# Optimization experiments

Measured on AMD Instinct MI355X. Metric: run time of the kernel, lower is better.

## Reference

```python
import jax, jax.numpy as jnp
import numpy as np

EPS = 1.1920928955078125e-07  # torch fp32 default eps for F.rms_norm
N_HEADS = 16
HEAD_DIM = 128


def apply_rotary_emb(x, cos, sin):
    # x: [B,S,H,D]; cos/sin: [1,S,1,D/2]
    d = x.shape[-1] // 2
    x1, x2 = x[..., :d], x[..., d:]
    return jnp.concatenate([x1 * cos + x2 * sin, -x1 * sin + x2 * cos], axis=-1)


def rms_norm(x):
    # F.rms_norm over last dim, no learned weight
    ms = jnp.mean(jnp.square(x), axis=-1, keepdims=True)
    return x * jax.lax.rsqrt(ms + EPS)


def setup_inputs() -> dict:
    key = jax.random.key(0)
    ks = jax.random.split(key, 7)
    B, S, D = 2, 2048, 2048
    half = HEAD_DIM // 2
    # rotary tables (built like standard RoPE for realism)
    inv_freq = 1.0 / (10000.0 ** (np.arange(0, half, dtype=np.float32) / half))
    t = np.arange(S, dtype=np.float32)
    freqs = np.outer(t, inv_freq)  # [S, D/2]
    cos = jnp.asarray(np.cos(freqs))[None, :, None, :]
    sin = jnp.asarray(np.sin(freqs))[None, :, None, :]
    sd = 1.0 / np.sqrt(D)
    return {
        "x": jax.random.normal(ks[0], (B, S, D), jnp.float32),
        "cos": cos,
        "sin": sin,
        "Wq": jax.random.normal(ks[1], (D, D), jnp.float32) * sd,
        "Wk": jax.random.normal(ks[2], (D, D), jnp.float32) * sd,
        "Wv": jax.random.normal(ks[3], (D, D), jnp.float32) * sd,
        "Wo": jax.random.normal(ks[4], (D, D), jnp.float32) * sd,
    }


def reference(x, cos, sin, Wq, Wk, Wv, Wo):
    B, S, D = x.shape
    H, Hd = N_HEADS, HEAD_DIM
    q = (x @ Wq.T).reshape(B, S, H, Hd)
    k = (x @ Wk.T).reshape(B, S, H, Hd)
    v = (x @ Wv.T).reshape(B, S, H, Hd)
    q = apply_rotary_emb(q, cos[:, :S], sin[:, :S])
    k = apply_rotary_emb(k, cos[:, :S], sin[:, :S])
    q = rms_norm(q) * 1.2  # [B,S,H,Hd]
    k = rms_norm(k) * 1.2
    scale = 1.0 / jnp.sqrt(jnp.asarray(Hd, x.dtype))
    # scores: [B,H,Sq,Sk]
    scores = jnp.einsum("bqhd,bkhd->bhqk", q, k) * scale
    attn = jax.nn.softmax(scores, axis=-1)
    y = jnp.einsum("bhqk,bkhd->bqhd", attn, v).reshape(B, S, D)
    return y @ Wo.T
```

## Files before the change

kernel.cpp:

```cpp
#include <hip/hip_runtime.h>
#include <hip/hip_bf16.h>
#include <math.h>

typedef __bf16 bf16;
typedef __attribute__((ext_vector_type(8))) __bf16 bf16x8;
typedef __attribute__((ext_vector_type(4))) float f32x4;

#define DEV __device__ __forceinline__

DEV void gload16(const void* g, void* l) {
    __builtin_amdgcn_global_load_lds(
        (__attribute__((address_space(1))) void*)(void*)g,
        (__attribute__((address_space(3))) void*)l, 16, 0, 0);
}

DEV unsigned pk2(float a, float b) {
    union { bf16 h[2]; unsigned u; } z;
    z.h[0] = (bf16)a; z.h[1] = (bf16)b;
    return z.u;
}

__global__ __launch_bounds__(256) void cvt_kernel(const float* __restrict__ in,
                                                  bf16* __restrict__ out, int n8) {
    for (int i = blockIdx.x * 256 + threadIdx.x; i < n8; i += gridDim.x * 256) {
        const float4* p = (const float4*)(in + (size_t)i * 8);
        float4 a = p[0], b = p[1];
        bf16x8 o;
        o[0] = (bf16)a.x; o[1] = (bf16)a.y; o[2] = (bf16)a.z; o[3] = (bf16)a.w;
        o[4] = (bf16)b.x; o[5] = (bf16)b.y; o[6] = (bf16)b.z; o[7] = (bf16)b.w;
        *(bf16x8*)(out + (size_t)i * 8) = o;
    }
}

template <bool F32OUT>
__global__ __launch_bounds__(256) void gemm_bt(const bf16* __restrict__ A,
                                               const bf16* __restrict__ B,
                                               void* __restrict__ Cout,
                                               int M, int N, int K) {
    __shared__ __align__(16) bf16 As[128 * 64];
    __shared__ __align__(16) bf16 Bs[128 * 64];
    const int tid = threadIdx.x, lane = tid & 63, wv = tid >> 6;
    const int tm = blockIdx.y * 128, tn = blockIdx.x * 128;
    const int wr = (wv >> 1) * 64, wc = (wv & 1) * 64;

    f32x4 acc[4][4] = {};
    const int scb = (lane & 7) * 16;

    for (int k0 = 0; k0 < K; k0 += 64) {
#pragma unroll
        for (int i = 0; i < 4; ++i) {
            int chunk = wv * 4 + i;
            int row = chunk * 8 + (lane >> 3);
            int cb = scb ^ ((row & 7) << 4);
            gload16((const char*)(A + (size_t)(tm + row) * K + k0) + cb,
                    (char*)As + chunk * 1024);
            gload16((const char*)(B + (size_t)(tn + row) * K + k0) + cb,
                    (char*)Bs + chunk * 1024);
        }
        __syncthreads();
#pragma unroll
        for (int kk = 0; kk < 2; ++kk) {
            bf16x8 af[4], bfr[4];
#pragma unroll
            for (int m = 0; m < 4; ++m) {
                int row = wr + m * 16 + (lane & 15);
                int cb = (kk * 64 + ((lane >> 4) * 16)) ^ ((row & 7) << 4);
                af[m] = *(const bf16x8*)((const char*)As + row * 128 + cb);
            }
#pragma unroll
            for (int n = 0; n < 4; ++n) {
                int row = wc + n * 16 + (lane & 15);
                int cb = (kk * 64 + ((lane >> 4) * 16)) ^ ((row & 7) << 4);
                bfr[n] = *(const bf16x8*)((const char*)Bs + row * 128 + cb);
            }
#pragma unroll
            for (int m = 0; m < 4; ++m)
#pragma unroll
                for (int n = 0; n < 4; ++n)
                    acc[m][n] = __builtin_amdgcn_mfma_f32_16x16x32_bf16(
                        af[m], bfr[n], acc[m][n], 0, 0, 0);
        }
        __syncthreads();
    }
#pragma unroll
    for (int m = 0; m < 4; ++m)
#pragma unroll
        for (int n = 0; n < 4; ++n)
#pragma unroll
            for (int r = 0; r < 4; ++r) {
                int row = tm + wr + m * 16 + (lane >> 4) * 4 + r;
                int col = tn + wc + n * 16 + (lane & 15);
                if (F32OUT)
                    ((float*)Cout)[(size_t)row * N + col] = acc[m][n][r];
                else
                    ((bf16*)Cout)[(size_t)row * N + col] = (bf16)acc[m][n][r];
            }
}

__global__ __launch_bounds__(256) void rope_rms(bf16* __restrict__ q,
                                                bf16* __restrict__ k,
                                                const float* __restrict__ cosp,
                                                const float* __restrict__ sinp) {
    int gw = blockIdx.x * 4 + (threadIdx.x >> 6);
    int lane = threadIdx.x & 63;
    bf16* base = (blockIdx.y == 0) ? q : k;
    int m = gw >> 4, h = gw & 15;
    int s = m & 2047;
    bf16* p = base + (size_t)m * 2048 + h * 128;
    float x1 = (float)p[lane], x2 = (float)p[lane + 64];
    float c = cosp[s * 64 + lane], si = sinp[s * 64 + lane];
    float r1 = x1 * c + x2 * si;
    float r2 = x2 * c - x1 * si;
    float ss = r1 * r1 + r2 * r2;
#pragma unroll
    for (int msk = 1; msk < 64; msk <<= 1) ss += __shfl_xor(ss, msk);
    float sc = rsqrtf(ss * (1.0f / 128.0f) + 1.1920928955078125e-07f) * 1.2f;
    p[lane] = (bf16)(r1 * sc);
    p[lane + 64] = (bf16)(r2 * sc);
}

__global__ __launch_bounds__(512) void attn_kernel(const bf16* __restrict__ q,
                                                   const bf16* __restrict__ k,
                                                   const bf16* __restrict__ v,
                                                   bf16* __restrict__ y) {
    __shared__ __align__(16) bf16 Ks[64 * 128];
    __shared__ __align__(16) bf16 Vt[128][72];

    const int tid = threadIdx.x, lane = tid & 63, wv = tid >> 6;
    const int hi = lane >> 4, ql = lane & 15;

    int wgid = blockIdx.y * 16 + blockIdx.x;
    int xcd = wgid & 7, j = wgid >> 3;
    int bh = xcd * 4 + (j >> 4);
    int qblk = j & 15;
    const int b = bh >> 4, h = bh & 15;
    const int q0 = qblk * 128;

    const bf16* qrow = q + (size_t)(b * 2048 + q0 + wv * 16 + ql) * 2048 +
                       h * 128 + hi * 8;
    bf16x8 qf[4];
#pragma unroll
    for (int kk = 0; kk < 4; ++kk) qf[kk] = *(const bf16x8*)(qrow + kk * 32);

    float mrun = -INFINITY, lrun = 0.f;
    f32x4 acco[8] = {};

    const int dcol = lane + 64 * (wv & 1);
    const int kvg = wv >> 1;
    const bf16* vcol = v + (size_t)(b * 2048) * 2048 + h * 128 + dcol;

    const float scale = 0.08838834764831845f;

    for (int kt = 0; kt < 2048; kt += 64) {
#pragma unroll
        for (int i = 0; i < 2; ++i) {
            int chunk = wv * 2 + i;
            int row = chunk * 4 + hi;
            int cb = ((lane & 15) * 16) ^ ((row & 7) << 4);
            gload16((const char*)(k + (size_t)(b * 2048 + kt + row) * 2048 + h * 128) + cb,
                    (char*)Ks + chunk * 1024);
        }
        {
            const bf16* vp = vcol + (size_t)(kt + kvg * 16) * 2048;
            bf16x8 va, vb2;
#pragma unroll
            for (int jj = 0; jj < 8; ++jj) {
                va[jj] = vp[(size_t)jj * 2048];
                vb2[jj] = vp[(size_t)(jj + 8) * 2048];
            }
            *(bf16x8*)(&Vt[dcol][kvg * 16]) = va;
            *(bf16x8*)(&Vt[dcol][kvg * 16 + 8]) = vb2;
        }
        __syncthreads();

        f32x4 st[4];
#pragma unroll
        for (int kc = 0; kc < 4; ++kc) {
            f32x4 a = {};
#pragma unroll
            for (int kk = 0; kk < 4; ++kk) {
                int row = kc * 16 + ql;
                int cb = (kk * 64 + 16 * hi) ^ ((row & 7) << 4);
                const bf16x8 kf = *(const bf16x8*)((const char*)Ks + row * 256 + cb);
                a = __builtin_amdgcn_mfma_f32_16x16x32_bf16(kf, qf[kk], a, 0, 0, 0);
            }
            st[kc] = a;
        }

        float s[4][4], mx = -INFINITY;
#pragma unroll
        for (int kc = 0; kc < 4; ++kc)
#pragma unroll
            for (int r = 0; r < 4; ++r) {
                s[kc][r] = st[kc][r] * scale;
                mx = fmaxf(mx, s[kc][r]);
            }
        mx = fmaxf(mx, __shfl_xor(mx, 16));
        mx = fmaxf(mx, __shfl_xor(mx, 32));
        float mn = fmaxf(mrun, mx);
        float alpha = __expf(mrun - mn);
        mrun = mn;
        float p[4][4], rs = 0.f;
#pragma unroll
        for (int kc = 0; kc < 4; ++kc)
#pragma unroll
            for (int r = 0; r < 4; ++r) {
                p[kc][r] = __expf(s[kc][r] - mn);
                rs += p[kc][r];
            }
        rs += __shfl_xor(rs, 16);
        rs += __shfl_xor(rs, 32);
        lrun = lrun * alpha + rs;

        float al[4];
#pragma unroll
        for (int r = 0; r < 4; ++r) al[r] = __shfl(alpha, hi * 4 + r);
#pragma unroll
        for (int dc = 0; dc < 8; ++dc) {
            acco[dc][0] *= al[0];
            acco[dc][1] *= al[1];
            acco[dc][2] *= al[2];
            acco[dc][3] *= al[3];
        }

        unsigned pk[4][2];
#pragma unroll
        for (int kc = 0; kc < 4; ++kc) {
            pk[kc][0] = pk2(p[kc][0], p[kc][1]);
            pk[kc][1] = pk2(p[kc][2], p[kc][3]);
        }

        const int s1 = ql + 16 * (2 * (hi & 1));
        const int s2 = s1 + 16;
        const bool up = hi >= 2;
#pragma unroll
        for (int kk2 = 0; kk2 < 2; ++kk2) {
            unsigned A0 = (unsigned)__shfl((int)pk[2 * kk2][0], s1);
            unsigned A1 = (unsigned)__shfl((int)pk[2 * kk2][1], s1);
            unsigned B0 = (unsigned)__shfl((int)pk[2 * kk2 + 1][0], s1);
            unsigned B1 = (unsigned)__shfl((int)pk[2 * kk2 + 1][1], s1);
            unsigned C0 = (unsigned)__shfl((int)pk[2 * kk2][0], s2);
            unsigned C1 = (unsigned)__shfl((int)pk[2 * kk2][1], s2);
            unsigned D0 = (unsigned)__shfl((int)pk[2 * kk2 + 1][0], s2);
            unsigned D1 = (unsigned)__shfl((int)pk[2 * kk2 + 1][1], s2);
            union { unsigned u[4]; bf16x8 v; } fr;
            fr.u[0] = up ? B0 : A0;
            fr.u[1] = up ? B1 : A1;
            fr.u[2] = up ? D0 : C0;
            fr.u[3] = up ? D1 : C1;
            const bf16x8 pa = fr.v;
#pragma unroll
            for (int dc = 0; dc < 8; ++dc) {
                const bf16x8 vf = *(const bf16x8*)(&Vt[dc * 16 + ql][kk2 * 32 + hi * 8]);
                acco[dc] = __builtin_amdgcn_mfma_f32_16x16x32_bf16(pa, vf, acco[dc], 0, 0, 0);
            }
        }
        __syncthreads();
    }

    float linv = 1.0f / lrun;
    float il[4];
#pragma unroll
    for (int r = 0; r < 4; ++r) il[r] = __shfl(linv, hi * 4 + r);
#pragma unroll
    for (int dc = 0; dc < 8; ++dc)
#pragma unroll
        for (int r = 0; r < 4; ++r) {
            int row = q0 + wv * 16 + hi * 4 + r;
            int col = h * 128 + dc * 16 + ql;
            y[(size_t)(b * 2048 + row) * 2048 + col] = (bf16)(acco[dc][r] * il[r]);
        }
}

extern "C" void kernel_launch(void* const* d_in, const int* in_sizes, int n_in,
                              void* d_out, int out_size, void* d_ws, size_t ws_size,
                              hipStream_t stream) {
    const float* x = (const float*)d_in[0];
    const float* cs = (const float*)d_in[1];
    const float* sn = (const float*)d_in[2];
    const float* Wq = (const float*)d_in[3];
    const float* Wk = (const float*)d_in[4];
    const float* Wv = (const float*)d_in[5];
    const float* Wo = (const float*)d_in[6];

    char* ws = (char*)d_ws;
    bf16* xb  = (bf16*)(ws + 0);
    bf16* wqb = (bf16*)(ws + 16777216);
    bf16* wkb = (bf16*)(ws + 25165824);
    bf16* wvb = (bf16*)(ws + 33554432);
    bf16* wob = (bf16*)(ws + 41943040);
    bf16* qb  = (bf16*)(ws + 50331648);
    bf16* kb  = (bf16*)(ws + 67108864);
    bf16* vb  = (bf16*)(ws + 83886080);
    bf16* yb  = (bf16*)(ws + 100663296);

    cvt_kernel<<<1024, 256, 0, stream>>>(x, xb, 8388608 / 8);
    cvt_kernel<<<512, 256, 0, stream>>>(Wq, wqb, 4194304 / 8);
    cvt_kernel<<<512, 256, 0, stream>>>(Wk, wkb, 4194304 / 8);
    cvt_kernel<<<512, 256, 0, stream>>>(Wv, wvb, 4194304 / 8);
    cvt_kernel<<<512, 256, 0, stream>>>(Wo, wob, 4194304 / 8);

    dim3 g(16, 32);
    gemm_bt<false><<<g, 256, 0, stream>>>(xb, wqb, qb, 4096, 2048, 2048);
    gemm_bt<false><<<g, 256, 0, stream>>>(xb, wkb, kb, 4096, 2048, 2048);
    gemm_bt<false><<<g, 256, 0, stream>>>(xb, wvb, vb, 4096, 2048, 2048);

    rope_rms<<<dim3(16384, 2), 256, 0, stream>>>(qb, kb, cs, sn);

    attn_kernel<<<dim3(16, 32), 512, 0, stream>>>(qb, kb, vb, yb);

    gemm_bt<true><<<g, 256, 0, stream>>>(yb, wob, d_out, 4096, 2048, 2048);
}
```

Baseline: 351.8 us.

## Restructure attention around 32x32 MFMA with lazy softmax rescaling

The attention kernel moves from 16x16x32 to 32x32x16 MFMA tiles, with 4 waves of 32 query rows each instead of 8 waves of 16. It uses v_permlane32_swap to rebuild the P operand instead of many shuffles. The softmax scale and log2(e) are folded into Q in the rope kernel so exp2f can be used, and output rescaling only happens when the running max grows by more than 8. V is loaded as paired bf16 words, and setprio is raised around the MFMA phases. The goal is fewer shuffle and VALU instructions per tile and higher MFMA efficiency, at the cost of more registers per thread, fewer threads per block, and a threshold-based rescale that changes when accumulators are normalized.

```diff
diff --git a/kernel.cpp b/kernel.cpp
--- a/kernel.cpp
+++ b/kernel.cpp
@@ -5,6 +5,7 @@
 typedef __bf16 bf16;
 typedef __attribute__((ext_vector_type(8))) __bf16 bf16x8;
 typedef __attribute__((ext_vector_type(4))) float f32x4;
+typedef __attribute__((ext_vector_type(16))) float f32x16;
 
 #define DEV __device__ __forceinline__
 
@@ -18,6 +19,10 @@
     union { bf16 h[2]; unsigned u; } z;
     z.h[0] = (bf16)a; z.h[1] = (bf16)b;
     return z.u;
+}
+
+DEV void plswap(unsigned& a, unsigned& b) {
+    asm volatile("v_permlane32_swap_b32 %0, %1" : "+v"(a), "+v"(b));
 }
 
 __global__ __launch_bounds__(256) void cvt_kernel(const float* __restrict__ in,
@@ -115,19 +120,20 @@
 #pragma unroll
     for (int msk = 1; msk < 64; msk <<= 1) ss += __shfl_xor(ss, msk);
     float sc = rsqrtf(ss * (1.0f / 128.0f) + 1.1920928955078125e-07f) * 1.2f;
+    if (blockIdx.y == 0) sc *= (0.08838834764831845f * 1.4426950408889634f);
     p[lane] = (bf16)(r1 * sc);
     p[lane + 64] = (bf16)(r2 * sc);
 }
 
-__global__ __launch_bounds__(512) void attn_kernel(const bf16* __restrict__ q,
-                                                   const bf16* __restrict__ k,
-                                                   const bf16* __restrict__ v,
-                                                   bf16* __restrict__ y) {
+__global__ __launch_bounds__(256, 3) void attn_kernel(const bf16* __restrict__ q,
+                                                      const bf16* __restrict__ k,
+                                                      const bf16* __restrict__ v,
+                                                      bf16* __restrict__ y) {
     __shared__ __align__(16) bf16 Ks[64 * 128];
     __shared__ __align__(16) bf16 Vt[128][72];
 
     const int tid = threadIdx.x, lane = tid & 63, wv = tid >> 6;
-    const int hi = lane >> 4, ql = lane & 15;
+    const int q31 = lane & 31, h5 = lane >> 5;
 
     int wgid = blockIdx.y * 16 + blockIdx.x;
     int xcd = wgid & 7, j = wgid >> 3;
@@ -136,140 +142,136 @@
     const int b = bh >> 4, h = bh & 15;
     const int q0 = qblk * 128;
 
-    const bf16* qrow = q + (size_t)(b * 2048 + q0 + wv * 16 + ql) * 2048 +
-                       h * 128 + hi * 8;
-    bf16x8 qf[4];
-#pragma unroll
-    for (int kk = 0; kk < 4; ++kk) qf[kk] = *(const bf16x8*)(qrow + kk * 32);
+    const bf16* qptr = q + (size_t)(b * 2048 + q0 + wv * 32 + q31) * 2048 +
+                       h * 128 + h5 * 8;
+    bf16x8 qf[8];
+#pragma unroll
+    for (int ks = 0; ks < 8; ++ks) qf[ks] = *(const bf16x8*)(qptr + ks * 16);
 
     float mrun = -INFINITY, lrun = 0.f;
-    f32x4 acco[8] = {};
-
-    const int dcol = lane + 64 * (wv & 1);
-    const int kvg = wv >> 1;
-    const bf16* vcol = v + (size_t)(b * 2048) * 2048 + h * 128 + dcol;
-
-    const float scale = 0.08838834764831845f;
+    f32x16 acco[4] = {};
+
+    const bf16* vbase = v + (size_t)(b * 2048 + wv * 16) * 2048 + h * 128 + 2 * lane;
+    const bf16* kbase = k + (size_t)(b * 2048) * 2048 + h * 128;
 
     for (int kt = 0; kt < 2048; kt += 64) {
 #pragma unroll
-        for (int i = 0; i < 2; ++i) {
-            int chunk = wv * 2 + i;
-            int row = chunk * 4 + hi;
+        for (int i = 0; i < 4; ++i) {
+            int chunk = wv * 4 + i;
+            int row = chunk * 4 + (lane >> 4);
             int cb = ((lane & 15) * 16) ^ ((row & 7) << 4);
-            gload16((const char*)(k + (size_t)(b * 2048 + kt + row) * 2048 + h * 128) + cb,
+            gload16((const char*)(kbase + (size_t)(kt + row) * 2048) + cb,
                     (char*)Ks + chunk * 1024);
         }
         {
-            const bf16* vp = vcol + (size_t)(kt + kvg * 16) * 2048;
-            bf16x8 va, vb2;
+            const bf16* vp = vbase + (size_t)kt * 2048;
+            unsigned u[16];
+#pragma unroll
+            for (int jj = 0; jj < 16; ++jj)
+                u[jj] = *(const unsigned*)(vp + (size_t)jj * 2048);
+            union { unsigned short s[8]; bf16x8 v8; } r0a, r0b, r1a, r1b;
 #pragma unroll
             for (int jj = 0; jj < 8; ++jj) {
-                va[jj] = vp[(size_t)jj * 2048];
-                vb2[jj] = vp[(size_t)(jj + 8) * 2048];
-            }
-            *(bf16x8*)(&Vt[dcol][kvg * 16]) = va;
-            *(bf16x8*)(&Vt[dcol][kvg * 16 + 8]) = vb2;
+                r0a.s[jj] = (unsigned short)(u[jj] & 0xffff);
+                r1a.s[jj] = (unsigned short)(u[jj] >> 16);
+                r0b.s[jj] = (unsigned short)(u[jj + 8] & 0xffff);
+                r1b.s[jj] = (unsigned short)(u[jj + 8] >> 16);
+            }
+            *(bf16x8*)(&Vt[2 * lane][wv * 16]) = r0a.v8;
+            *(bf16x8*)(&Vt[2 * lane][wv * 16 + 8]) = r0b.v8;
+            *(bf16x8*)(&Vt[2 * lane + 1][wv * 16]) = r1a.v8;
+            *(bf16x8*)(&Vt[2 * lane + 1][wv * 16 + 8]) = r1b.v8;
         }
         __syncthreads();
 
-        f32x4 st[4];
-#pragma unroll
-        for (int kc = 0; kc < 4; ++kc) {
-            f32x4 a = {};
-#pragma unroll
-            for (int kk = 0; kk < 4; ++kk) {
-                int row = kc * 16 + ql;
-                int cb = (kk * 64 + 16 * hi) ^ ((row & 7) << 4);
+        f32x16 st[2];
+        __builtin_amdgcn_s_setprio(1);
+#pragma unroll
+        for (int kvb = 0; kvb < 2; ++kvb) {
+            f32x16 a = {};
+#pragma unroll
+            for (int ks = 0; ks < 8; ++ks) {
+                int row = kvb * 32 + q31;
+                int cb = (32 * ks + 16 * h5) ^ ((row & 7) << 4);
                 const bf16x8 kf = *(const bf16x8*)((const char*)Ks + row * 256 + cb);
-                a = __builtin_amdgcn_mfma_f32_16x16x32_bf16(kf, qf[kk], a, 0, 0, 0);
-            }
-            st[kc] = a;
-        }
-
-        float s[4][4], mx = -INFINITY;
-#pragma unroll
-        for (int kc = 0; kc < 4; ++kc)
-#pragma unroll
-            for (int r = 0; r < 4; ++r) {
-                s[kc][r] = st[kc][r] * scale;
-                mx = fmaxf(mx, s[kc][r]);
-            }
-        mx = fmaxf(mx, __shfl_xor(mx, 16));
+                a = __builtin_amdgcn_mfma_f32_32x32x16_bf16(kf, qf[ks], a, 0, 0, 0);
+            }
+            st[kvb] = a;
+        }
+        __builtin_amdgcn_s_setprio(0);
+
+        float t8[8];
+#pragma unroll
+        for (int r = 0; r < 8; ++r)
+            t8[r] = fmaxf(fmaxf(st[0][r], st[0][r + 8]),
+                          fmaxf(st[1][r], st[1][r + 8]));
+        float mx = fmaxf(fmaxf(fmaxf(t8[0], t8[1]), fmaxf(t8[2], t8[3])),
+                         fmaxf(fmaxf(t8[4], t8[5]), fmaxf(t8[6], t8[7])));
         mx = fmaxf(mx, __shfl_xor(mx, 32));
-        float mn = fmaxf(mrun, mx);
-        float alpha = __expf(mrun - mn);
-        mrun = mn;
-        float p[4][4], rs = 0.f;
-#pragma unroll
-        for (int kc = 0; kc < 4; ++kc)
-#pragma unroll
-            for (int r = 0; r < 4; ++r) {
-                p[kc][r] = __expf(s[kc][r] - mn);
-                rs += p[kc][r];
-            }
-        rs += __shfl_xor(rs, 16);
+
+        if (__any(mx - mrun > 8.0f)) {
+            float mn = fmaxf(mrun, mx);
+            float alpha = exp2f(mrun - mn);
+            mrun = mn;
+            lrun *= alpha;
+#pragma unroll
+            for (int r = 0; r < 16; ++r) {
+                int qr = (r & 3) + 8 * (r >> 2) + 4 * h5;
+                float al = __shfl(alpha, qr);
+                acco[0][r] *= al; acco[1][r] *= al;
+                acco[2][r] *= al; acco[3][r] *= al;
+            }
+        }
+
+        unsigned w[2][8];
+        float rsa = 0.f, rsb = 0.f;
+#pragma unroll
+        for (int kvb = 0; kvb < 2; ++kvb)
+#pragma unroll
+            for (int i = 0; i < 8; ++i) {
+                float p0 = exp2f(st[kvb][2 * i] - mrun);
+                float p1 = exp2f(st[kvb][2 * i + 1] - mrun);
+                if (i & 1) rsb += p0 + p1; else rsa += p0 + p1;
+                w[kvb][i] = pk2(p0, p1);
+            }
+        float rs = rsa + rsb;
         rs += __shfl_xor(rs, 32);
-        lrun = lrun * alpha + rs;
-
-        float al[4];
-#pragma unroll
-        for (int r = 0; r < 4; ++r) al[r] = __shfl(alpha, hi * 4 + r);
-#pragma unroll
-        for (int dc = 0; dc < 8; ++dc) {
-            acco[dc][0] *= al[0];
-            acco[dc][1] *= al[1];
-            acco[dc][2] *= al[2];
-            acco[dc][3] *= al[3];
-        }
-
-        unsigned pk[4][2];
-#pragma unroll
-        for (int kc = 0; kc < 4; ++kc) {
-            pk[kc][0] = pk2(p[kc][0], p[kc][1]);
-            pk[kc][1] = pk2(p[kc][2], p[kc][3]);
-        }
-
-        const int s1 = ql + 16 * (2 * (hi & 1));
-        const int s2 = s1 + 16;
-        const bool up = hi >= 2;
-#pragma unroll
-        for (int kk2 = 0; kk2 < 2; ++kk2) {
-            unsigned A0 = (unsigned)__shfl((int)pk[2 * kk2][0], s1);
-            unsigned A1 = (unsigned)__shfl((int)pk[2 * kk2][1], s1);
-            unsigned B0 = (unsigned)__shfl((int)pk[2 * kk2 + 1][0], s1);
-            unsigned B1 = (unsigned)__shfl((int)pk[2 * kk2 + 1][1], s1);
-            unsigned C0 = (unsigned)__shfl((int)pk[2 * kk2][0], s2);
-            unsigned C1 = (unsigned)__shfl((int)pk[2 * kk2][1], s2);
-            unsigned D0 = (unsigned)__shfl((int)pk[2 * kk2 + 1][0], s2);
-            unsigned D1 = (unsigned)__shfl((int)pk[2 * kk2 + 1][1], s2);
-            union { unsigned u[4]; bf16x8 v; } fr;
-            fr.u[0] = up ? B0 : A0;
-            fr.u[1] = up ? B1 : A1;
-            fr.u[2] = up ? D0 : C0;
-            fr.u[3] = up ? D1 : C1;
-            const bf16x8 pa = fr.v;
-#pragma unroll
-            for (int dc = 0; dc < 8; ++dc) {
-                const bf16x8 vf = *(const bf16x8*)(&Vt[dc * 16 + ql][kk2 * 32 + hi * 8]);
-                acco[dc] = __builtin_amdgcn_mfma_f32_16x16x32_bf16(pa, vf, acco[dc], 0, 0, 0);
-            }
-        }
+        lrun += rs;
+
+        __builtin_amdgcn_s_setprio(1);
+#pragma unroll
+        for (int b2 = 0; b2 < 2; ++b2)
+#pragma unroll
+            for (int ksl = 0; ksl < 2; ++ksl) {
+                const int ks = b2 * 2 + ksl, u0 = ksl * 4;
+                unsigned f0 = w[b2][u0 + 0], f2 = w[b2][u0 + 2];
+                unsigned f1 = w[b2][u0 + 1], f3 = w[b2][u0 + 3];
+                plswap(f0, f2);
+                plswap(f1, f3);
+                union { unsigned uu[4]; bf16x8 v8; } fr;
+                fr.uu[0] = f0; fr.uu[1] = f1; fr.uu[2] = f2; fr.uu[3] = f3;
+#pragma unroll
+                for (int dblk = 0; dblk < 4; ++dblk) {
+                    const bf16x8 vf =
+                        *(const bf16x8*)(&Vt[dblk * 32 + q31][ks * 16 + h5 * 8]);
+                    acco[dblk] = __builtin_amdgcn_mfma_f32_32x32x16_bf16(
+                        fr.v8, vf, acco[dblk], 0, 0, 0);
+                }
+            }
+        __builtin_amdgcn_s_setprio(0);
         __syncthreads();
     }
 
     float linv = 1.0f / lrun;
-    float il[4];
-#pragma unroll
-    for (int r = 0; r < 4; ++r) il[r] = __shfl(linv, hi * 4 + r);
-#pragma unroll
-    for (int dc = 0; dc < 8; ++dc)
-#pragma unroll
-        for (int r = 0; r < 4; ++r) {
-            int row = q0 + wv * 16 + hi * 4 + r;
-            int col = h * 128 + dc * 16 + ql;
-            y[(size_t)(b * 2048 + row) * 2048 + col] = (bf16)(acco[dc][r] * il[r]);
-        }
+#pragma unroll
+    for (int r = 0; r < 16; ++r) {
+        int qr = (r & 3) + 8 * (r >> 2) + 4 * h5;
+        float il = __shfl(linv, qr);
+        size_t row = (size_t)(b * 2048 + q0 + wv * 32 + qr) * 2048 + h * 128;
+#pragma unroll
+        for (int dblk = 0; dblk < 4; ++dblk)
+            y[row + dblk * 32 + q31] = (bf16)(acco[dblk][r] * il);
+    }
 }
 
 extern "C" void kernel_launch(void* const* d_in, const int* in_sizes, int n_in,
@@ -307,7 +309,7 @@
 
     rope_rms<<<dim3(16384, 2), 256, 0, stream>>>(qb, kb, cs, sn);
 
-    attn_kernel<<<dim3(16, 32), 512, 0, stream>>>(qb, kb, vb, yb);
+    attn_kernel<<<dim3(16, 32), 256, 0, stream>>>(qb, kb, vb, yb);
 
     gemm_bt<true><<<g, 256, 0, stream>>>(yb, wob, d_out, 4096, 2048, 2048);
 }
```

After: 345.2 us. No clear change (-1.9%).
